# Kernel optimization log

Measured on AMD Instinct MI355X. Metric: run time of the kernel, lower is better.

## Reference

```python
import jax, jax.numpy as jnp
import numpy as np

B, N, H, W, C_OUT = 4, 480000, 1024, 1024, 64
PR = (0.0, -39.68, -3.0, 69.12, 39.68, 1.0)  # point cloud range [x0,y0,z0,x1,y1,z1]
BN_EPS = 1e-5


def setup_inputs():
    key = jax.random.key(0)
    ks = iter(jax.random.split(key, 48))
    bidx = jax.random.randint(next(ks), (N,), 0, B).astype(jnp.float32)
    px = jax.random.uniform(next(ks), (N,), minval=PR[0], maxval=PR[3])
    py = jax.random.uniform(next(ks), (N,), minval=PR[1], maxval=PR[4])
    pz = jax.random.uniform(next(ks), (N,), minval=PR[2], maxval=PR[5])
    pi = jax.random.uniform(next(ks), (N,))
    points = jnp.stack([bidx, px, py, pz, pi], axis=1)  # [N,5]

    def w(shape):
        return jax.random.normal(next(ks), shape, jnp.float32) * 0.1

    def bnp(c):
        return (1.0 + 0.1 * jax.random.normal(next(ks), (c,), jnp.float32),
                0.1 * jax.random.normal(next(ks), (c,), jnp.float32),
                0.1 * jax.random.normal(next(ks), (c,), jnp.float32),
                jax.random.uniform(next(ks), (c,), minval=0.5, maxval=1.5))

    g0, be0, m0, v0 = bnp(8)
    g1, be1, m1, v1 = bnp(16)
    g2, be2, m2, v2 = bnp(32)
    g3, be3, m3, v3 = bnp(C_OUT)
    return {
        'points': points, 'batch_size': B,
        'w0': w((8, 2, 3, 3)), 'b0': w((8,)),
        'g0': g0, 'be0': be0, 'm0': m0, 'v0': v0,
        'w1': w((16, 1, 3, 3)), 'b1': w((16,)),  # groups=8 conv: 16 out, 8 in groups
        'g1': g1, 'be1': be1, 'm1': m1, 'v1': v1,
        'wdw': w((16, 1, 3, 3)), 'bdw': w((16,)),
        'wpw': w((32, 16, 1, 1)), 'bpw': w((32,)),
        'g2': g2, 'be2': be2, 'm2': m2, 'v2': v2,
        'w3': w((C_OUT, 32, 3, 3)), 'b3': w((C_OUT,)),
        'g3': g3, 'be3': be3, 'm3': m3, 'v3': v3,
    }


def conv2d(x, wt, b, groups=1, pad=1):
    out = jax.lax.conv_general_dilated(
        x, wt, (1, 1), [(pad, pad), (pad, pad)],
        feature_group_count=groups,
        dimension_numbers=('NCHW', 'OIHW', 'NCHW'))
    return out + b[None, :, None, None]


def bn(x, g, be, m, v):
    s = g * jax.lax.rsqrt(v + BN_EPS)
    return x * s[None, :, None, None] + (be - m * s)[None, :, None, None]


def maxpool2(x):
    return jax.lax.reduce_window(x, -jnp.inf, jax.lax.max,
                                 (1, 1, 2, 2), (1, 1, 2, 2), 'VALID')


def channel_shuffle(x, groups):
    b, c, h, w = x.shape
    return x.reshape(b, groups, c // groups, h, w).transpose(0, 2, 1, 3, 4).reshape(b, c, h, w)


def rasterize(points, batch_size):
    # points: [N,5] = (batch_idx, x, y, z, intensity)
    x_scale = W / (PR[3] - PR[0])
    y_scale = H / (PR[4] - PR[1])
    # PR[0]==0 -> no x shift (matches the source's branch)
    xp = (points[:, 1] * x_scale).astype(jnp.int32)  # trunc toward zero like torch .to(int)
    yp = ((points[:, 2] + (PR[4] - PR[1]) / 2) * y_scale).astype(jnp.int32)
    valid = (xp >= 0) & (xp < W) & (yp >= 0) & (yp < H)
    bi = jnp.where(valid, points[:, 0].astype(jnp.int32), batch_size)  # invalid -> OOB, dropped
    xi = jnp.where(valid, xp, W)
    yi = jnp.where(valid, yp, H)
    bev_z = jnp.full((batch_size, H, W), -10.0, jnp.float32)
    bev_z = bev_z.at[bi, yi, xi].max(points[:, 3], mode='drop')
    bev_i = jnp.zeros((batch_size, H, W), jnp.float32)
    bev_i = bev_i.at[bi, yi, xi].max(points[:, 4], mode='drop')
    return jnp.stack([bev_z, bev_i], axis=1)  # [B,2,H,W]


def reference(points, batch_size, w0, b0, g0, be0, m0, v0, w1, b1, g1, be1, m1, v1,
              wdw, bdw, wpw, bpw, g2, be2, m2, v2, w3, b3, g3, be3, m3, v3):
    x = rasterize(points, batch_size)
    x = jax.nn.relu(bn(conv2d(x, w0, b0), g0, be0, m0, v0))          # x_conv1
    x = maxpool2(x)
    x = jax.nn.relu(bn(conv2d(x, w1, b1, groups=8), g1, be1, m1, v1))  # x_conv2
    x = maxpool2(x)
    x = conv2d(x, wdw, bdw, groups=16)      # depthwise
    x = channel_shuffle(x, 16)              # identity when groups==channels, kept for faithfulness
    x = conv2d(x, wpw, bpw, pad=0)          # pointwise 16->32
    x = jax.nn.relu(bn(x, g2, be2, m2, v2))
    x = jax.nn.relu(bn(conv2d(x, w3, b3), g3, be3, m3, v3))          # x_conv3
    x = maxpool2(x)                         # x_conv4 == spatial_features
    return x
```

## Files before the change

### kernel.cpp

```cpp
#include <hip/hip_runtime.h>
#include <cstddef>

#define H_IN 1024
#define W_IN 1024
#define BN_EPS 1e-5f

typedef float f32x4 __attribute__((ext_vector_type(4)));
typedef _Float16 f16x8 __attribute__((ext_vector_type(8)));

__device__ __forceinline__ unsigned encF(float f) {
    unsigned u = __float_as_uint(f);
    return (u & 0x80000000u) ? ~u : (u | 0x80000000u);
}
__device__ __forceinline__ float decF(unsigned e, float untouched) {
    if (e == 0u) return untouched;
    unsigned bits = (e & 0x80000000u) ? (e ^ 0x80000000u) : ~e;
    return __uint_as_float(bits);
}

__global__ void k_rasterize(const float* __restrict__ pts, unsigned* __restrict__ bev, int n) {
    int i = blockIdx.x * blockDim.x + threadIdx.x;
    if (i >= n) return;
    float fb  = pts[(size_t)i*5+0];
    float px  = pts[(size_t)i*5+1];
    float py  = pts[(size_t)i*5+2];
    float pz  = pts[(size_t)i*5+3];
    float pit = pts[(size_t)i*5+4];
    const float XS = (float)(1024.0/69.12);
    const float YS = (float)(1024.0/79.36);
    int xp = (int)(px * XS);
    int yp = (int)((py + 39.68f) * YS);
    if (xp < 0 || xp >= W_IN || yp < 0 || yp >= H_IN) return;
    int b = (int)fb;
    size_t off = (((size_t)b * H_IN + yp) * W_IN + xp) * 2;
    atomicMax(bev + off,     encF(pz));
    atomicMax(bev + off + 1, encF(pit));
}

__global__ __launch_bounds__(256, 4) void k_conv1(
                        const unsigned* __restrict__ bev, const float* __restrict__ w0,
                        const float* __restrict__ b0, const float* __restrict__ g0,
                        const float* __restrict__ be0, const float* __restrict__ m0,
                        const float* __restrict__ v0, _Float16* __restrict__ out) {
    __shared__ float wS[144];
    __shared__ float sS[8], tS[8];
    int t = threadIdx.x;
    if (t < 144) wS[t] = w0[t];
    if (t < 8) {
        float s = g0[t] / sqrtf(v0[t] + BN_EPS);
        sS[t] = s;
        tS[t] = (b0[t] - m0[t]) * s + be0[t];
    }
    __syncthreads();
    int idx = blockIdx.x * 256 + t;
    int x = idx & 511, y = (idx >> 9) & 511, b = idx >> 18;
    const unsigned* base = bev + (size_t)b * H_IN * W_IN * 2;
    float in[2][4][4];
    #pragma unroll
    for (int r = 0; r < 4; r++) {
        int iy = 2*y - 1 + r;
        #pragma unroll
        for (int cc = 0; cc < 4; cc++) {
            int ix = 2*x - 1 + cc;
            if (iy >= 0 && iy < H_IN && ix >= 0 && ix < W_IN) {
                const unsigned* p2 = base + ((size_t)iy*W_IN + ix)*2;
                in[0][r][cc] = decF(p2[0], -10.0f);
                in[1][r][cc] = decF(p2[1], 0.0f);
            } else {
                in[0][r][cc] = 0.0f;
                in[1][r][cc] = 0.0f;
            }
        }
    }
    f16x8 ov;
    #pragma unroll
    for (int oc = 0; oc < 8; oc++) {
        float mx = 0.0f;
        #pragma unroll
        for (int py = 0; py < 2; py++)
            #pragma unroll
            for (int px = 0; px < 2; px++) {
                float acc = 0.0f;
                #pragma unroll
                for (int c = 0; c < 2; c++)
                    #pragma unroll
                    for (int kh = 0; kh < 3; kh++)
                        #pragma unroll
                        for (int kw = 0; kw < 3; kw++)
                            acc += in[c][py+kh][px+kw] * wS[((oc*2+c)*3+kh)*3+kw];
                acc = fmaxf(acc * sS[oc] + tS[oc], 0.0f);
                mx = fmaxf(mx, acc);
            }
        ov[oc] = (_Float16)mx;
    }
    *(f16x8*)(out + ((size_t)((b*512 + y)*512 + x)) * 8) = ov;
}

__global__ __launch_bounds__(256, 4) void k_conv2(
                        const _Float16* __restrict__ x1, const float* __restrict__ w1,
                        const float* __restrict__ b1, const float* __restrict__ g1,
                        const float* __restrict__ be1, const float* __restrict__ m1,
                        const float* __restrict__ v1, float* __restrict__ out) {
    __shared__ float wS[144];
    __shared__ float sS[16], tS[16];
    int t = threadIdx.x;
    if (t < 144) wS[t] = w1[t];
    if (t < 16) {
        float s = g1[t] / sqrtf(v1[t] + BN_EPS);
        sS[t] = s;
        tS[t] = (b1[t] - m1[t]) * s + be1[t];
    }
    __syncthreads();
    int idx = blockIdx.x * 256 + t;
    int x = idx & 255, y = (idx >> 8) & 255, b = idx >> 16;
    const _Float16* base = x1 + (size_t)b * 512 * 512 * 8;

    f16x8 p[4][4];
    #pragma unroll
    for (int r = 0; r < 4; r++) {
        int iy = 2*y - 1 + r;
        #pragma unroll
        for (int c = 0; c < 4; c++) {
            int ix = 2*x - 1 + c;
            if (iy >= 0 && iy < 512 && ix >= 0 && ix < 512) {
                p[r][c] = *(const f16x8*)(base + ((size_t)iy*512 + ix)*8);
            } else {
                f16x8 z = {0,0,0,0,0,0,0,0};
                p[r][c] = z;
            }
        }
    }

    float* ob = out + (size_t)b * 16 * 256 * 256 + (size_t)y*256 + x;
    #pragma unroll
    for (int g = 0; g < 8; g++) {
        #pragma unroll
        for (int sub = 0; sub < 2; sub++) {
            int oc = g*2 + sub;
            float mx = 0.0f;
            #pragma unroll
            for (int qy = 0; qy < 2; qy++)
                #pragma unroll
                for (int qx = 0; qx < 2; qx++) {
                    float acc = 0.0f;
                    #pragma unroll
                    for (int kh = 0; kh < 3; kh++)
                        #pragma unroll
                        for (int kw = 0; kw < 3; kw++)
                            acc += (float)p[qy+kh][qx+kw][g] * wS[(oc*3+kh)*3+kw];
                    acc = fmaxf(acc * sS[oc] + tS[oc], 0.0f);
                    mx = fmaxf(mx, acc);
                }
            ob[(size_t)oc*65536] = mx;
        }
    }
}

__global__ __launch_bounds__(256, 4) void k_dwpw(
                       const float* __restrict__ x2, const float* __restrict__ wdw,
                       const float* __restrict__ bdw, const float* __restrict__ wpw,
                       const float* __restrict__ bpw, const float* __restrict__ g2,
                       const float* __restrict__ be2, const float* __restrict__ m2,
                       const float* __restrict__ v2, _Float16* __restrict__ out) {
    __shared__ float patch[16*10*36];
    __shared__ float wdwS[144];
    __shared__ float bdwS[16];
    __shared__ float wpwS[512];
    __shared__ float sS[32], tS[32];
    int t = threadIdx.x;
    if (t < 144) wdwS[t] = wdw[t];
    if (t < 16) bdwS[t] = bdw[t];
    for (int i = t; i < 512; i += 256) wpwS[i] = wpw[i];
    if (t < 32) {
        float s = g2[t] / sqrtf(v2[t] + BN_EPS);
        sS[t] = s;
        tS[t] = (bpw[t] - m2[t]) * s + be2[t];
    }

    int bi = blockIdx.x;
    int tx = bi & 7, ty = (bi >> 3) & 31, b = bi >> 8;
    int x0 = tx * 32, y0 = ty * 8;
    const float* base = x2 + (size_t)b * 16 * 256 * 256;

    for (int i = t; i < 16*10*34; i += 256) {
        int ic = i / 340;
        int rem = i - ic * 340;
        int r = rem / 34, c = rem - r * 34;
        int gy = y0 - 1 + r, gx = x0 - 1 + c;
        patch[(ic*10 + r)*36 + c] =
            (gy >= 0 && gy < 256 && gx >= 0 && gx < 256)
                ? base[(size_t)ic*65536 + (size_t)gy*256 + gx] : 0.0f;
    }
    __syncthreads();

    int px = t & 31, pyy = t >> 5;
    int x = x0 + px, y = y0 + pyy;

    float dv[16];
    #pragma unroll
    for (int ic = 0; ic < 16; ic++) {
        float d = bdwS[ic];
        #pragma unroll
        for (int r = 0; r < 3; r++)
            #pragma unroll
            for (int c = 0; c < 3; c++)
                d += patch[(ic*10 + pyy + r)*36 + px + c] * wdwS[ic*9 + r*3 + c];
        dv[ic] = d;
    }

    _Float16* ob = out + ((size_t)((b*256 + y)*256 + x)) * 32;
    #pragma unroll
    for (int q = 0; q < 4; q++) {
        f16x8 ov;
        #pragma unroll
        for (int j = 0; j < 8; j++) {
            int oc = q*8 + j;
            float a = 0.0f;
            #pragma unroll
            for (int ic = 0; ic < 16; ic++)
                a += dv[ic] * wpwS[oc*16+ic];
            ov[j] = (_Float16)fmaxf(a*sS[oc] + tS[oc], 0.0f);
        }
        *(f16x8*)(ob + q*8) = ov;
    }
}

__global__ void k_wprep(const float* __restrict__ w3, const float* __restrict__ b3,
                        const float* __restrict__ g3, const float* __restrict__ be3,
                        const float* __restrict__ m3, const float* __restrict__ v3,
                        _Float16* __restrict__ wh, float* __restrict__ tv) {
    __shared__ float sSh[64];
    int t = threadIdx.x;
    if (t < 64) {
        float s = g3[t] / sqrtf(v3[t] + BN_EPS);
        sSh[t] = s;
        if (blockIdx.x == 0) tv[t] = (b3[t] - m3[t]) * s + be3[t];
    }
    __syncthreads();
    int khw = blockIdx.x;
    for (int i = t; i < 2048; i += 256) {
        int oc = i >> 5;
        wh[khw*2048 + i] = (_Float16)(w3[(size_t)i*9 + khw] * sSh[oc]);
    }
}

__global__ __launch_bounds__(256, 2) void k_conv3m(const _Float16* __restrict__ xh,
                                                   const _Float16* __restrict__ wh,
                                                   const float* __restrict__ tv,
                                                   float* __restrict__ out) {
    __shared__ _Float16 As[10*66*40];
    int t = threadIdx.x;
    int lane = t & 63, w = t >> 6;
    int l15 = lane & 15, l4 = lane >> 4;
    int bi = blockIdx.x;
    int xt = bi & 3, yg = (bi >> 2) & 31, b = bi >> 7;
    int x0 = xt * 64;
    int y0 = yg * 8;

    f16x8 Bf[9][4];
    #pragma unroll
    for (int khw = 0; khw < 9; khw++)
        #pragma unroll
        for (int g = 0; g < 4; g++)
            Bf[khw][g] = *(const f16x8*)(wh + ((khw*64 + g*16 + l15)*32 + 8*l4));

    float tvv[4];
    #pragma unroll
    for (int g = 0; g < 4; g++) tvv[g] = tv[g*16 + l15];

    for (int s = t; s < 660; s += 256) {
        int row = s / 66, px = s - row*66;
        int gy = y0 - 1 + row, gx = x0 - 1 + px;
        float4* dst = (float4*)&As[(row*66 + px)*40];
        if (gy >= 0 && gy < 256 && gx >= 0 && gx < 256) {
            const float4* src = (const float4*)(xh + ((size_t)((b*256 + gy)*256 + gx)) * 32);
            #pragma unroll
            for (int j = 0; j < 4; j++) dst[j] = src[j];
        } else {
            float4 z = make_float4(0.f, 0.f, 0.f, 0.f);
            #pragma unroll
            for (int j = 0; j < 4; j++) dst[j] = z;
        }
    }
    __syncthreads();

    for (int ti = 0; ti < 4; ti++) {
        int ypool = yg*4 + ti;
        f32x4 acc[2][4];
        #pragma unroll
        for (int f = 0; f < 2; f++)
            #pragma unroll
            for (int g = 0; g < 4; g++)
                acc[f][g] = (f32x4){0.f, 0.f, 0.f, 0.f};

        #pragma unroll
        for (int kh = 0; kh < 3; kh++)
            #pragma unroll
            for (int kw = 0; kw < 3; kw++) {
                f16x8 Af[2];
                #pragma unroll
                for (int f = 0; f < 2; f++) {
                    int row = 2*ti + f + kh;
                    int px = w*16 + l15 + kw;
                    Af[f] = *(const f16x8*)&As[(row*66 + px)*40 + 8*l4];
                }
                #pragma unroll
                for (int f = 0; f < 2; f++)
                    #pragma unroll
                    for (int g = 0; g < 4; g++)
                        acc[f][g] = __builtin_amdgcn_mfma_f32_16x16x32_f16(
                            Af[f], Bf[kh*3+kw][g], acc[f][g], 0, 0, 0);
            }

        #pragma unroll
        for (int g = 0; g < 4; g++) {
            int oc = g*16 + l15;
            #pragma unroll
            for (int q = 0; q < 2; q++) {
                float v0 = fmaxf(fmaxf(acc[0][g][2*q]   + tvv[g], 0.f),
                                 fmaxf(acc[0][g][2*q+1] + tvv[g], 0.f));
                float v1 = fmaxf(fmaxf(acc[1][g][2*q]   + tvv[g], 0.f),
                                 fmaxf(acc[1][g][2*q+1] + tvv[g], 0.f));
                int px = x0/2 + w*8 + 2*l4 + q;
                out[(((size_t)b*64 + oc)*128 + ypool)*128 + px] = fmaxf(v0, v1);
            }
        }
    }
}

extern "C" void kernel_launch(void* const* d_in, const int* in_sizes, int n_in,
                              void* d_out, int out_size, void* d_ws, size_t ws_size,
                              hipStream_t stream) {
    const float* points = (const float*)d_in[0];
    int n = in_sizes[0] / 5;
    const float* w0  = (const float*)d_in[2];
    const float* b0  = (const float*)d_in[3];
    const float* g0  = (const float*)d_in[4];
    const float* be0 = (const float*)d_in[5];
    const float* m0  = (const float*)d_in[6];
    const float* v0  = (const float*)d_in[7];
    const float* w1  = (const float*)d_in[8];
    const float* b1  = (const float*)d_in[9];
    const float* g1  = (const float*)d_in[10];
    const float* be1 = (const float*)d_in[11];
    const float* m1  = (const float*)d_in[12];
    const float* v1  = (const float*)d_in[13];
    const float* wdw = (const float*)d_in[14];
    const float* bdw = (const float*)d_in[15];
    const float* wpw = (const float*)d_in[16];
    const float* bpw = (const float*)d_in[17];
    const float* g2  = (const float*)d_in[18];
    const float* be2 = (const float*)d_in[19];
    const float* m2  = (const float*)d_in[20];
    const float* v2  = (const float*)d_in[21];
    const float* w3  = (const float*)d_in[22];
    const float* b3  = (const float*)d_in[23];
    const float* g3  = (const float*)d_in[24];
    const float* be3 = (const float*)d_in[25];
    const float* m3  = (const float*)d_in[26];
    const float* v3  = (const float*)d_in[27];

    float* ws  = (float*)d_ws;
    unsigned* bev = (unsigned*)ws;
    _Float16* x1h = (_Float16*)(ws + 8388608);
    float* x2  = ws;
    _Float16* x3h = (_Float16*)(ws + 8388608);
    _Float16* wh  = (_Float16*)(ws + 16777216);
    float* tv  = ws + 16786432;
    float* outp = (float*)d_out;

    k_wprep<<<9, 256, 0, stream>>>(w3, b3, g3, be3, m3, v3, wh, tv);
    hipMemsetAsync(bev, 0, (size_t)4 * H_IN * W_IN * 2 * sizeof(unsigned), stream);
    k_rasterize<<<(n + 255)/256, 256, 0, stream>>>(points, bev, n);
    k_conv1<<<4096, 256, 0, stream>>>(bev, w0, b0, g0, be0, m0, v0, x1h);
    k_conv2<<<1024, 256, 0, stream>>>(x1h, w1, b1, g1, be1, m1, v1, x2);
    k_dwpw<<<1024, 256, 0, stream>>>(x2, wdw, bdw, wpw, bpw, g2, be2, m2, v2, x3h);
    k_conv3m<<<512, 256, 0, stream>>>(x3h, wh, tv, outp);
}
```

Baseline: 142.2 us.

## Fuse conv2+pool into depthwise/pointwise kernel and merge memset with weight prep

Fuses the grouped conv2 + BN + ReLU + maxpool stage into the depthwise/pointwise kernel. Each block loads a halo tile of x1 into shared memory, computes the pooled x2 tile (with its 1-pixel halo) in LDS, then runs the dw/pw conv from LDS, removing the fp32 x2 round trip through global memory and one launch. It also replaces the hipMemset plus the weight-prep kernel with a single kernel that zeroes the BEV buffer and prepares the conv3 weights. In exchange, x2 halo pixels are recomputed, only 340 of 256 threads' worth of work exists in the conv2 phase (poor thread utilization), and shared memory use goes up, lowering occupancy.

Result: no change. 139.4 us (-1.9%).

```diff
diff --git a/kernel.cpp b/kernel.cpp
--- a/kernel.cpp
+++ b/kernel.cpp
@@ -16,6 +16,35 @@
     if (e == 0u) return untouched;
     unsigned bits = (e & 0x80000000u) ? (e ^ 0x80000000u) : ~e;
     return __uint_as_float(bits);
+}
+
+__global__ void k_prep(uint4* __restrict__ bevq,
+                       const float* __restrict__ w3, const float* __restrict__ b3,
+                       const float* __restrict__ g3, const float* __restrict__ be3,
+                       const float* __restrict__ m3, const float* __restrict__ v3,
+                       _Float16* __restrict__ wh, float* __restrict__ tv) {
+    int bid = blockIdx.x;
+    int t = threadIdx.x;
+    if (bid < 2048) {
+        int i = bid * 256 + t;
+        uint4 z = {0u, 0u, 0u, 0u};
+        #pragma unroll
+        for (int j = 0; j < 4; j++)
+            bevq[(size_t)j*524288 + i] = z;
+        return;
+    }
+    __shared__ float sSh[64];
+    if (t < 64) {
+        float s = g3[t] / sqrtf(v3[t] + BN_EPS);
+        sSh[t] = s;
+        if (bid == 2048) tv[t] = (b3[t] - m3[t]) * s + be3[t];
+    }
+    __syncthreads();
+    int khw = bid - 2048;
+    for (int i = t; i < 2048; i += 256) {
+        int oc = i >> 5;
+        wh[khw*2048 + i] = (_Float16)(w3[(size_t)i*9 + khw] * sSh[oc]);
+    }
 }
 
 __global__ void k_rasterize(const float* __restrict__ pts, unsigned* __restrict__ bev, int n) {
@@ -96,106 +125,87 @@
     *(f16x8*)(out + ((size_t)((b*512 + y)*512 + x)) * 8) = ov;
 }
 
-__global__ __launch_bounds__(256, 4) void k_conv2(
-                        const _Float16* __restrict__ x1, const float* __restrict__ w1,
-                        const float* __restrict__ b1, const float* __restrict__ g1,
-                        const float* __restrict__ be1, const float* __restrict__ m1,
-                        const float* __restrict__ v1, float* __restrict__ out) {
-    __shared__ float wS[144];
-    __shared__ float sS[16], tS[16];
+__global__ __launch_bounds__(256, 3) void k_conv2dw(
+        const _Float16* __restrict__ x1,
+        const float* __restrict__ w1, const float* __restrict__ b1,
+        const float* __restrict__ g1, const float* __restrict__ be1,
+        const float* __restrict__ m1, const float* __restrict__ v1,
+        const float* __restrict__ wdw, const float* __restrict__ bdw,
+        const float* __restrict__ wpw, const float* __restrict__ bpw,
+        const float* __restrict__ g2, const float* __restrict__ be2,
+        const float* __restrict__ m2, const float* __restrict__ v2,
+        _Float16* __restrict__ out) {
+    __shared__ _Float16 x1S[8][22][72];
+    __shared__ float x2S[16][10][36];
+    __shared__ float w1S[144], s1S[16], t1S[16];
+    __shared__ float wdwS[144], bdwS[16], wpwS[512], s2S[32], t2S[32];
     int t = threadIdx.x;
-    if (t < 144) wS[t] = w1[t];
+    if (t < 144) { w1S[t] = w1[t]; wdwS[t] = wdw[t]; }
     if (t < 16) {
         float s = g1[t] / sqrtf(v1[t] + BN_EPS);
-        sS[t] = s;
-        tS[t] = (b1[t] - m1[t]) * s + be1[t];
-    }
-    __syncthreads();
-    int idx = blockIdx.x * 256 + t;
-    int x = idx & 255, y = (idx >> 8) & 255, b = idx >> 16;
-    const _Float16* base = x1 + (size_t)b * 512 * 512 * 8;
-
-    f16x8 p[4][4];
-    #pragma unroll
-    for (int r = 0; r < 4; r++) {
-        int iy = 2*y - 1 + r;
-        #pragma unroll
-        for (int c = 0; c < 4; c++) {
-            int ix = 2*x - 1 + c;
-            if (iy >= 0 && iy < 512 && ix >= 0 && ix < 512) {
-                p[r][c] = *(const f16x8*)(base + ((size_t)iy*512 + ix)*8);
-            } else {
-                f16x8 z = {0,0,0,0,0,0,0,0};
-                p[r][c] = z;
-            }
-        }
-    }
-
-    float* ob = out + (size_t)b * 16 * 256 * 256 + (size_t)y*256 + x;
-    #pragma unroll
-    for (int g = 0; g < 8; g++) {
-        #pragma unroll
-        for (int sub = 0; sub < 2; sub++) {
-            int oc = g*2 + sub;
-            float mx = 0.0f;
-            #pragma unroll
-            for (int qy = 0; qy < 2; qy++)
-                #pragma unroll
-                for (int qx = 0; qx < 2; qx++) {
-                    float acc = 0.0f;
-                    #pragma unroll
-                    for (int kh = 0; kh < 3; kh++)
-                        #pragma unroll
-                        for (int kw = 0; kw < 3; kw++)
-                            acc += (float)p[qy+kh][qx+kw][g] * wS[(oc*3+kh)*3+kw];
-                    acc = fmaxf(acc * sS[oc] + tS[oc], 0.0f);
-                    mx = fmaxf(mx, acc);
-                }
-            ob[(size_t)oc*65536] = mx;
-        }
-    }
-}
-
-__global__ __launch_bounds__(256, 4) void k_dwpw(
-                       const float* __restrict__ x2, const float* __restrict__ wdw,
-                       const float* __restrict__ bdw, const float* __restrict__ wpw,
-                       const float* __restrict__ bpw, const float* __restrict__ g2,
-                       const float* __restrict__ be2, const float* __restrict__ m2,
-                       const float* __restrict__ v2, _Float16* __restrict__ out) {
-    __shared__ float patch[16*10*36];
-    __shared__ float wdwS[144];
-    __shared__ float bdwS[16];
-    __shared__ float wpwS[512];
-    __shared__ float sS[32], tS[32];
-    int t = threadIdx.x;
-    if (t < 144) wdwS[t] = wdw[t];
-    if (t < 16) bdwS[t] = bdw[t];
+        s1S[t] = s; t1S[t] = (b1[t] - m1[t]) * s + be1[t];
+        bdwS[t] = bdw[t];
+    }
     for (int i = t; i < 512; i += 256) wpwS[i] = wpw[i];
     if (t < 32) {
         float s = g2[t] / sqrtf(v2[t] + BN_EPS);
-        sS[t] = s;
-        tS[t] = (bpw[t] - m2[t]) * s + be2[t];
-    }
-
+        s2S[t] = s; t2S[t] = (bpw[t] - m2[t]) * s + be2[t];
+    }
     int bi = blockIdx.x;
     int tx = bi & 7, ty = (bi >> 3) & 31, b = bi >> 8;
     int x0 = tx * 32, y0 = ty * 8;
-    const float* base = x2 + (size_t)b * 16 * 256 * 256;
-
-    for (int i = t; i < 16*10*34; i += 256) {
-        int ic = i / 340;
-        int rem = i - ic * 340;
-        int r = rem / 34, c = rem - r * 34;
+
+    const _Float16* base1 = x1 + (size_t)b * 512 * 512 * 8;
+    int ry0 = 2*y0 - 3, cx0 = 2*x0 - 3;
+    for (int i = t; i < 22*70; i += 256) {
+        int r = i / 70, c = i - r*70;
+        int gy = ry0 + r, gx = cx0 + c;
+        f16x8 v = {0,0,0,0,0,0,0,0};
+        if (gy >= 0 && gy < 512 && gx >= 0 && gx < 512)
+            v = *(const f16x8*)(base1 + ((size_t)gy*512 + gx)*8);
+        #pragma unroll
+        for (int j = 0; j < 8; j++)
+            x1S[j][r][c] = v[j];
+    }
+    __syncthreads();
+
+    for (int i = t; i < 340; i += 256) {
+        int r = i / 34, c = i - r*34;
         int gy = y0 - 1 + r, gx = x0 - 1 + c;
-        patch[(ic*10 + r)*36 + c] =
-            (gy >= 0 && gy < 256 && gx >= 0 && gx < 256)
-                ? base[(size_t)ic*65536 + (size_t)gy*256 + gx] : 0.0f;
+        bool valid = (gy >= 0 && gy < 256 && gx >= 0 && gx < 256);
+        #pragma unroll
+        for (int g = 0; g < 8; g++) {
+            float p[4][4];
+            #pragma unroll
+            for (int rr = 0; rr < 4; rr++)
+                #pragma unroll
+                for (int cc = 0; cc < 4; cc++)
+                    p[rr][cc] = (float)x1S[g][2*r + rr][2*c + cc];
+            #pragma unroll
+            for (int sub = 0; sub < 2; sub++) {
+                int oc = g*2 + sub;
+                float mx = 0.0f;
+                #pragma unroll
+                for (int qy = 0; qy < 2; qy++)
+                    #pragma unroll
+                    for (int qx = 0; qx < 2; qx++) {
+                        float acc = 0.0f;
+                        #pragma unroll
+                        for (int kh = 0; kh < 3; kh++)
+                            #pragma unroll
+                            for (int kw = 0; kw < 3; kw++)
+                                acc += p[qy+kh][qx+kw] * w1S[(oc*3+kh)*3+kw];
+                        acc = fmaxf(acc * s1S[oc] + t1S[oc], 0.0f);
+                        mx = fmaxf(mx, acc);
+                    }
+                x2S[oc][r][c] = valid ? mx : 0.0f;
+            }
+        }
     }
     __syncthreads();
 
     int px = t & 31, pyy = t >> 5;
     int x = x0 + px, y = y0 + pyy;
-
     float dv[16];
     #pragma unroll
     for (int ic = 0; ic < 16; ic++) {
@@ -204,10 +214,9 @@
         for (int r = 0; r < 3; r++)
             #pragma unroll
             for (int c = 0; c < 3; c++)
-                d += patch[(ic*10 + pyy + r)*36 + px + c] * wdwS[ic*9 + r*3 + c];
+                d += x2S[ic][pyy + r][px + c] * wdwS[ic*9 + r*3 + c];
         dv[ic] = d;
     }
-
     _Float16* ob = out + ((size_t)((b*256 + y)*256 + x)) * 32;
     #pragma unroll
     for (int q = 0; q < 4; q++) {
@@ -219,28 +228,9 @@
             #pragma unroll
             for (int ic = 0; ic < 16; ic++)
                 a += dv[ic] * wpwS[oc*16+ic];
-            ov[j] = (_Float16)fmaxf(a*sS[oc] + tS[oc], 0.0f);
+            ov[j] = (_Float16)fmaxf(a*s2S[oc] + t2S[oc], 0.0f);
         }
         *(f16x8*)(ob + q*8) = ov;
-    }
-}
-
-__global__ void k_wprep(const float* __restrict__ w3, const float* __restrict__ b3,
-                        const float* __restrict__ g3, const float* __restrict__ be3,
-                        const float* __restrict__ m3, const float* __restrict__ v3,
-                        _Float16* __restrict__ wh, float* __restrict__ tv) {
-    __shared__ float sSh[64];
-    int t = threadIdx.x;
-    if (t < 64) {
-        float s = g3[t] / sqrtf(v3[t] + BN_EPS);
-        sSh[t] = s;
-        if (blockIdx.x == 0) tv[t] = (b3[t] - m3[t]) * s + be3[t];
-    }
-    __syncthreads();
-    int khw = blockIdx.x;
-    for (int i = t; i < 2048; i += 256) {
-        int oc = i >> 5;
-        wh[khw*2048 + i] = (_Float16)(w3[(size_t)i*9 + khw] * sSh[oc]);
     }
 }
 
@@ -363,17 +353,15 @@
     float* ws  = (float*)d_ws;
     unsigned* bev = (unsigned*)ws;
     _Float16* x1h = (_Float16*)(ws + 8388608);
-    float* x2  = ws;
-    _Float16* x3h = (_Float16*)(ws + 8388608);
+    _Float16* x3h = (_Float16*)ws;
     _Float16* wh  = (_Float16*)(ws + 16777216);
     float* tv  = ws + 16786432;
     float* outp = (float*)d_out;
 
-    k_wprep<<<9, 256, 0, stream>>>(w3, b3, g3, be3, m3, v3, wh, tv);
-    hipMemsetAsync(bev, 0, (size_t)4 * H_IN * W_IN * 2 * sizeof(unsigned), stream);
+    k_prep<<<2057, 256, 0, stream>>>((uint4*)bev, w3, b3, g3, be3, m3, v3, wh, tv);
     k_rasterize<<<(n + 255)/256, 256, 0, stream>>>(points, bev, n);
     k_conv1<<<4096, 256, 0, stream>>>(bev, w0, b0, g0, be0, m0, v0, x1h);
-    k_conv2<<<1024, 256, 0, stream>>>(x1h, w1, b1, g1, be1, m1, v1, x2);
-    k_dwpw<<<1024, 256, 0, stream>>>(x2, wdw, bdw, wpw, bpw, g2, be2, m2, v2, x3h);
+    k_conv2dw<<<1024, 256, 0, stream>>>(x1h, w1, b1, g1, be1, m1, v1,
+                                        wdw, bdw, wpw, bpw, g2, be2, m2, v2, x3h);
     k_conv3m<<<512, 256, 0, stream>>>(x3h, wh, tv, outp);
 }
```
